# Kernel optimization log

Measured on AMD Instinct MI355X. Metric: run time of the kernel, lower is better.

## Reference

```python
import jax, jax.numpy as jnp
import numpy as np

B, S, D, H = 4, 2048, 512, 8
DH = D // H  # 64


def setup_inputs() -> dict:
    key = jax.random.key(0)
    ks = jax.random.split(key, 12)
    sc = 0.02
    return {
        "embed": jax.random.normal(ks[0], (B, S, D), dtype=jnp.float32),
        "Wq": jax.random.normal(ks[1], (H, DH, D), dtype=jnp.float32) * sc,
        "bq": jax.random.normal(ks[2], (H, DH), dtype=jnp.float32) * sc,
        "Wk": jax.random.normal(ks[3], (H, DH, D), dtype=jnp.float32) * sc,
        "bk": jax.random.normal(ks[4], (H, DH), dtype=jnp.float32) * sc,
        "Wv": jax.random.normal(ks[5], (H, DH, D), dtype=jnp.float32) * sc,
        "bv": jax.random.normal(ks[6], (H, DH), dtype=jnp.float32) * sc,
        "Wo": jax.random.normal(ks[7], (D, D), dtype=jnp.float32) * sc,
        "bo": jax.random.normal(ks[8], (D,), dtype=jnp.float32) * sc,
        "gamma": jnp.ones((D,), dtype=jnp.float32),
        "beta": jnp.zeros((D,), dtype=jnp.float32),
    }


def reference(embed, Wq, bq, Wk, bk, Wv, bv, Wo, bo, gamma, beta):
    # Per-head linear projections, vectorized over heads: [B,H,S,DH]
    q = jnp.einsum("bsd,hed->bhse", embed, Wq) + bq[None, :, None, :]
    k = jnp.einsum("bsd,hed->bhse", embed, Wk) + bk[None, :, None, :]
    v = jnp.einsum("bsd,hed->bhse", embed, Wv) + bv[None, :, None, :]

    # Full score matrix [B,H,S,S], tril applied to RAW scores (zeros, not -inf),
    # scaled by sqrt(embedding_dim) -- faithful to the original module's math.
    att = jnp.einsum("bhse,bhte->bhst", q, k)
    att = jnp.tril(att)
    att = att / jnp.sqrt(jnp.float32(D))
    att = jax.nn.softmax(att, axis=-1)

    out = jnp.einsum("bhst,bhte->bhse", att, v)  # [B,H,S,DH]
    # concat heads along feature dim -> [B,S,D]
    out = jnp.transpose(out, (0, 2, 1, 3)).reshape(B, S, D)

    x = out @ Wo.T + bo
    x = x + embed

    # LayerNorm over last dim
    mu = jnp.mean(x, axis=-1, keepdims=True)
    var = jnp.var(x, axis=-1, keepdims=True)
    x = (x - mu) / jnp.sqrt(var + 1e-5) * gamma + beta
    return x
```

## Files before the change

### kernel.cpp

```cpp
#include <hip/hip_runtime.h>
#include <hip/hip_bf16.h>


typedef __bf16 bf16;
typedef __bf16 bf16x8 __attribute__((ext_vector_type(8)));
typedef __bf16 bf16x4v __attribute__((ext_vector_type(4)));
typedef float f32x4 __attribute__((ext_vector_type(4)));

#define S_LEN 2048
#define DMODEL 512
#define QSCALE 0.06375870914f

#define GLDS(g, l) __builtin_amdgcn_global_load_lds(                  \
    (const __attribute__((address_space(1))) void*)(g),               \
    (__attribute__((address_space(3))) void*)(l), 16, 0, 0)

__global__ __launch_bounds__(256) void cast_all(
    const float* __restrict__ embed, const float* __restrict__ Wq,
    const float* __restrict__ Wk, const float* __restrict__ Wv,
    const float* __restrict__ Wo,
    bf16* __restrict__ Eb, bf16* __restrict__ Wqkv, bf16* __restrict__ Wob) {
  int i = blockIdx.x * 256 + threadIdx.x;
  const float* src;
  bf16* dst;
  int il;
  if (i < 1048576) {
    src = embed; dst = Eb; il = i;
  } else {
    int j = i - 1048576;
    int w = j >> 16;
    il = j & 65535;
    src = (w == 0) ? Wq : (w == 1) ? Wk : (w == 2) ? Wv : Wo;
    dst = (w == 3) ? Wob : Wqkv + (size_t)w * 262144;
  }
  float4 v = reinterpret_cast<const float4*>(src)[il];
  bf16x4v o;
  o[0] = (bf16)v.x; o[1] = (bf16)v.y; o[2] = (bf16)v.z; o[3] = (bf16)v.w;
  *reinterpret_cast<bf16x4v*>(dst + (size_t)il * 4) = o;
}

__device__ __forceinline__ void gemm128_core(
    const bf16* __restrict__ A, const bf16* __restrict__ Bw,
    int row0, int col0, bf16* As, bf16* Bs, f32x4 (&acc)[4][4]) {
  int tid = threadIdx.x;
  int w = tid >> 6, l = tid & 63, lr = l & 15, lg = l >> 4;
  int wr = w >> 1, wc = w & 1;

  int srow = w * 8 + (l >> 3);
  int scol = ((l & 7) ^ (srow & 7)) << 3;
  const bf16* ga = A + (size_t)(row0 + srow) * DMODEL + scol;
  const bf16* gb = Bw + (size_t)(col0 + srow) * DMODEL + scol;
  char* asb = (char*)As;
  char* bsb = (char*)Bs;
  int sbase = w * 1024;

  int aoff[4], boff[4];
#pragma unroll
  for (int m = 0; m < 4; ++m) {
    aoff[m] = (wr * 64 + m * 16 + lr) * 128 + (((lg ^ (lr & 7))) << 4);
    boff[m] = (wc * 64 + m * 16 + lr) * 128 + (((lg ^ (lr & 7))) << 4);
  }

  for (int k0 = 0; k0 < DMODEL; k0 += 64) {
#pragma unroll
    for (int qt = 0; qt < 4; ++qt) {
      GLDS(ga + (size_t)qt * 32 * DMODEL, asb + qt * 4096 + sbase);
      GLDS(gb + (size_t)qt * 32 * DMODEL, bsb + qt * 4096 + sbase);
    }
    ga += 64; gb += 64;
    __syncthreads();

    bf16x8 af[2][4], bfv[2][4];
#pragma unroll
    for (int m = 0; m < 4; ++m) {
      af[0][m] = *(const bf16x8*)(asb + aoff[m]);
      af[1][m] = *(const bf16x8*)(asb + (aoff[m] ^ 0x40));
      bfv[0][m] = *(const bf16x8*)(bsb + boff[m]);
      bfv[1][m] = *(const bf16x8*)(bsb + (boff[m] ^ 0x40));
    }
#pragma unroll
    for (int m = 0; m < 4; ++m)
#pragma unroll
      for (int n = 0; n < 4; ++n) {
        acc[m][n] = __builtin_amdgcn_mfma_f32_16x16x32_bf16(af[0][m], bfv[0][n], acc[m][n], 0, 0, 0);
        acc[m][n] = __builtin_amdgcn_mfma_f32_16x16x32_bf16(af[1][m], bfv[1][n], acc[m][n], 0, 0, 0);
      }
    __syncthreads();
  }
}

__global__ __launch_bounds__(256) void gemm_qkv(
    const bf16* __restrict__ A, const bf16* __restrict__ Wqkv,
    const float* __restrict__ bq, const float* __restrict__ bk, const float* __restrict__ bv,
    bf16* __restrict__ Qb, bf16* __restrict__ Kb, bf16* __restrict__ Vt) {
  __shared__ __align__(16) bf16 As[128 * 64];
  __shared__ __align__(16) bf16 Bs[128 * 64];
  int row0 = blockIdx.x * 128, col0 = blockIdx.y * 128;
  f32x4 acc[4][4] = {};
  gemm128_core(A, Wqkv, row0, col0, As, Bs, acc);

  int tid = threadIdx.x;
  int w = tid >> 6, l = tid & 63, lr = l & 15, lg = l >> 4;
  int wr = w >> 1, wc = w & 1;
  int z2 = col0 >> 9;
  if (z2 < 2) {
    bf16* O = z2 ? Kb : Qb;
    const float* bias = z2 ? bk : bq;
    float qs = z2 ? 1.0f : QSCALE;
#pragma unroll
    for (int n = 0; n < 4; ++n) {
      int cg = (col0 & 511) + wc * 64 + n * 16 + lr;
      float bi = bias[cg];
#pragma unroll
      for (int m = 0; m < 4; ++m) {
        int rg = row0 + wr * 64 + m * 16 + lg * 4;
#pragma unroll
        for (int r = 0; r < 4; ++r)
          O[(size_t)(rg + r) * DMODEL + cg] = (bf16)((acc[m][n][r] + bi) * qs);
      }
    }
  } else {
#pragma unroll
    for (int n = 0; n < 4; ++n) {
      int ep = (col0 & 511) + wc * 64 + n * 16 + lr;
      int h = ep >> 6, e = ep & 63;
      float bi = bv[ep];
#pragma unroll
      for (int m = 0; m < 4; ++m) {
        int rg = row0 + wr * 64 + m * 16 + lg * 4;
        int b = rg >> 11, s0 = rg & 2047;
        bf16x4v pk;
#pragma unroll
        for (int r = 0; r < 4; ++r) pk[r] = (bf16)(acc[m][n][r] + bi);
        *(bf16x4v*)(Vt + ((size_t)((b * 8 + h) * 64 + e)) * S_LEN + s0) = pk;
      }
    }
  }
}

__global__ __launch_bounds__(256) void gemm_wo(
    const bf16* __restrict__ A, const bf16* __restrict__ W,
    const float* __restrict__ bo, const float* __restrict__ embed,
    bf16* __restrict__ X) {
  __shared__ __align__(16) bf16 As[128 * 64];
  __shared__ __align__(16) bf16 Bs[128 * 64];
  int row0 = blockIdx.x * 128, col0 = blockIdx.y * 128;
  f32x4 acc[4][4] = {};
  gemm128_core(A, W, row0, col0, As, Bs, acc);

  int tid = threadIdx.x;
  int w = tid >> 6, l = tid & 63, lr = l & 15, lg = l >> 4;
  int wr = w >> 1, wc = w & 1;
#pragma unroll
  for (int n = 0; n < 4; ++n) {
    int cg = col0 + wc * 64 + n * 16 + lr;
    float bi = bo[cg];
#pragma unroll
    for (int m = 0; m < 4; ++m) {
      int rg = row0 + wr * 64 + m * 16 + lg * 4;
#pragma unroll
      for (int r = 0; r < 4; ++r)
        X[(size_t)(rg + r) * DMODEL + cg] =
            (bf16)(acc[m][n][r] + bi + embed[(size_t)(rg + r) * DMODEL + cg]);
    }
  }
}

__global__ __launch_bounds__(256) void suf_kernel(const bf16* __restrict__ Vt,
                                                  float* __restrict__ SUF) {
  int bh = blockIdx.x >> 3;
  int eg = blockIdx.x & 7;
  int el = threadIdx.x & 7;
  int seg = threadIdx.x >> 3;
  int e = eg * 8 + el;
  __shared__ float segtot[32][9];
  const bf16* vrow = Vt + ((size_t)bh * 64 + e) * S_LEN;
  float loc[4];
  float carry = 0.f;
#pragma unroll
  for (int j = 3; j >= 0; --j) {
    int jj = seg * 4 + j;
    bf16x8 a = *(const bf16x8*)(vrow + jj * 16);
    bf16x8 b2 = *(const bf16x8*)(vrow + jj * 16 + 8);
    float s = 0.f;
#pragma unroll
    for (int k = 0; k < 8; ++k) s += (float)a[k] + (float)b2[k];
    carry += s;
    loc[j] = carry;
  }
  segtot[seg][el] = carry;
  __syncthreads();
  float add = 0.f;
  for (int s2 = seg + 1; s2 < 32; ++s2) add += segtot[s2][el];
  float* srow = SUF + (size_t)bh * 129 * 64 + e;
#pragma unroll
  for (int j = 0; j < 4; ++j) srow[(size_t)(seg * 4 + j) * 64] = loc[j] + add;
  if (seg == 0) srow[(size_t)128 * 64] = 0.f;
}

__global__ __launch_bounds__(512) void flash_attn(
    const bf16* __restrict__ Qb, const bf16* __restrict__ Kb,
    const bf16* __restrict__ Vt, const float* __restrict__ SUF,
    bf16* __restrict__ attO) {
  int bh = blockIdx.y;
  int b = bh >> 3, h = bh & 7;
  int p = (int)gridDim.x - 1 - (int)blockIdx.x;
  int tid = threadIdx.x;
  int w = tid >> 6, l = tid & 63, lr = l & 15, lg = l >> 4;
  int wsub = w & 3;
  int qtile = (w < 4) ? (16 + p) : (15 - p);
  int qb = qtile * 64;
  int nt = 17 + p;

  __shared__ __align__(16) bf16 kl[3][64 * 64];
  __shared__ __align__(16) bf16 vl[3][64 * 64];
  __shared__ __align__(16) bf16 pl[8][16 * 64];

  int srow = qb + 16 * wsub + lr;
  const bf16* qptr = Qb + ((size_t)(b * S_LEN) + srow) * DMODEL + h * 64 + lg * 8;
  bf16x8 aq0 = *(const bf16x8*)(qptr);
  bf16x8 aq1 = *(const bf16x8*)(qptr + 32);

  float lsum[4] = {0.f, 0.f, 0.f, 0.f};
  f32x4 acc[4] = {};

  int tmax_w = qb + 16 * wsub + 16;

  int grow = tid >> 3, gch = tid & 7;
  int sch = ((gch ^ (grow & 7)) << 3);
  const bf16* Kg = Kb + ((size_t)(b * S_LEN) + grow) * DMODEL + h * 64 + sch;
  const bf16* Vg = Vt + ((size_t)(bh * 64) + grow) * S_LEN + sch;
  int sdst = w * 1024;

  int sw0 = (lg ^ (lr & 7)) << 4;
  int sw4 = sw0 ^ 0x40;
  char* plb = (char*)pl[w];

  GLDS(Kg, (char*)kl[0] + sdst);
  GLDS(Vg, (char*)vl[0] + sdst);
  GLDS(Kg + (size_t)64 * DMODEL, (char*)kl[1] + sdst);
  GLDS(Vg + 64, (char*)vl[1] + sdst);
  asm volatile("s_waitcnt vmcnt(2)" ::: "memory");
  __syncthreads();

  int cur = 0;
  for (int it = 0; it < nt; ++it) {
    int t0 = it << 6;
    bool more = (it + 2 < nt);
    if (more) {
      int stg = cur + 2; if (stg >= 3) stg -= 3;
      GLDS(Kg + (size_t)(t0 + 128) * DMODEL, (char*)kl[stg] + sdst);
      GLDS(Vg + (t0 + 128), (char*)vl[stg] + sdst);
    }
    if (t0 < tmax_w) {
      char* klb = (char*)kl[cur];
      char* vlb = (char*)vl[cur];

      f32x4 sfrag[4];
      const f32x4 fz = {0.f, 0.f, 0.f, 0.f};
      __builtin_amdgcn_s_setprio(1);
#pragma unroll
      for (int c = 0; c < 4; ++c) {
        int rb = (16 * c + lr) * 128;
        bf16x8 bk0 = *(const bf16x8*)(klb + rb + sw0);
        bf16x8 bk1 = *(const bf16x8*)(klb + rb + sw4);
        f32x4 t = __builtin_amdgcn_mfma_f32_16x16x32_bf16(aq0, bk0, fz, 0, 0, 0);
        sfrag[c] = __builtin_amdgcn_mfma_f32_16x16x32_bf16(aq1, bk1, t, 0, 0, 0);
      }
      __builtin_amdgcn_s_setprio(0);

      if (t0 + 64 <= qb + 16 * wsub) {
#pragma unroll
        for (int r = 0; r < 4; ++r) {
          int row = lg * 4 + r;
          int pbase = row * 128 + ((lr & 7) << 1);
          int xorv = row & 7;
          float psum = 0.f;
#pragma unroll
          for (int c = 0; c < 4; ++c) {
            float pv = exp2f(sfrag[c][r]);
            psum += pv;
            int chunk = 2 * c + (lr >> 3);
            *(bf16*)(plb + pbase + (((chunk ^ xorv) << 4))) = (bf16)pv;
          }
          lsum[r] += psum;
        }
      } else {
#pragma unroll
        for (int r = 0; r < 4; ++r) {
          int sg = qb + 16 * wsub + lg * 4 + r;
          int row = lg * 4 + r;
          int pbase = row * 128 + ((lr & 7) << 1);
          int xorv = row & 7;
          float psum = 0.f;
#pragma unroll
          for (int c = 0; c < 4; ++c) {
            int tg = t0 + 16 * c + lr;
            float x = (tg <= sg) ? sfrag[c][r] : ((tg < tmax_w) ? 0.f : -1e30f);
            float pv = exp2f(x);
            psum += pv;
            int chunk = 2 * c + (lr >> 3);
            *(bf16*)(plb + pbase + (((chunk ^ xorv) << 4))) = (bf16)pv;
          }
          lsum[r] += psum;
        }
      }

      bf16x8 pa0 = *(const bf16x8*)(plb + lr * 128 + sw0);
      bf16x8 pa1 = *(const bf16x8*)(plb + lr * 128 + sw4);
      __builtin_amdgcn_s_setprio(1);
#pragma unroll
      for (int c = 0; c < 4; ++c) {
        int rb = (16 * c + lr) * 128;
        bf16x8 bv0 = *(const bf16x8*)(vlb + rb + sw0);
        bf16x8 bv1 = *(const bf16x8*)(vlb + rb + sw4);
        acc[c] = __builtin_amdgcn_mfma_f32_16x16x32_bf16(pa0, bv0, acc[c], 0, 0, 0);
        acc[c] = __builtin_amdgcn_mfma_f32_16x16x32_bf16(pa1, bv1, acc[c], 0, 0, 0);
      }
      __builtin_amdgcn_s_setprio(0);
    }
    if (more) {
      asm volatile("s_waitcnt vmcnt(2)" ::: "memory");
    } else {
      asm volatile("s_waitcnt vmcnt(0)" ::: "memory");
    }
    __syncthreads();
    cur = (cur == 2) ? 0 : cur + 1;
  }

#pragma unroll
  for (int r = 0; r < 4; ++r) {
#pragma unroll
    for (int d = 1; d < 16; d <<= 1) lsum[r] += __shfl_xor(lsum[r], d, 64);
  }

  int j16 = tmax_w >> 4;
  const float* suf = SUF + ((size_t)bh * 129 + j16) * 64;
  float cnt = (float)(S_LEN - tmax_w);
  float sufe[4];
#pragma unroll
  for (int c = 0; c < 4; ++c) sufe[c] = suf[16 * c + lr];
#pragma unroll
  for (int r = 0; r < 4; ++r) {
    float inv = 1.f / (lsum[r] + cnt);
    int sg = qb + 16 * wsub + lg * 4 + r;
#pragma unroll
    for (int c = 0; c < 4; ++c) {
      float o = (acc[c][r] + sufe[c]) * inv;
      attO[((size_t)(b * S_LEN) + sg) * DMODEL + h * 64 + 16 * c + lr] = (bf16)o;
    }
  }
}

__global__ __launch_bounds__(256) void ln_kernel(const bf16* __restrict__ x,
                                                 const float* __restrict__ gamma,
                                                 const float* __restrict__ beta,
                                                 float* __restrict__ out) {
  int row = blockIdx.x * 4 + (threadIdx.x >> 6);
  int l = threadIdx.x & 63;
  bf16x8 xv = *(const bf16x8*)(x + (size_t)row * DMODEL + l * 8);
  float xf[8];
  float s = 0.f, s2 = 0.f;
#pragma unroll
  for (int k = 0; k < 8; ++k) {
    xf[k] = (float)xv[k];
    s += xf[k];
    s2 += xf[k] * xf[k];
  }
#pragma unroll
  for (int d = 1; d < 64; d <<= 1) {
    s += __shfl_xor(s, d, 64);
    s2 += __shfl_xor(s2, d, 64);
  }
  float mean = s * (1.f / 512.f);
  float var = s2 * (1.f / 512.f) - mean * mean;
  float rstd = rsqrtf(var + 1e-5f);
  const float4* g4 = reinterpret_cast<const float4*>(gamma) + l * 2;
  const float4* b4 = reinterpret_cast<const float4*>(beta) + l * 2;
  float4 g0 = g4[0], g1 = g4[1], bb0 = b4[0], bb1 = b4[1];
  float4 o0, o1;
  o0.x = (xf[0] - mean) * rstd * g0.x + bb0.x;
  o0.y = (xf[1] - mean) * rstd * g0.y + bb0.y;
  o0.z = (xf[2] - mean) * rstd * g0.z + bb0.z;
  o0.w = (xf[3] - mean) * rstd * g0.w + bb0.w;
  o1.x = (xf[4] - mean) * rstd * g1.x + bb1.x;
  o1.y = (xf[5] - mean) * rstd * g1.y + bb1.y;
  o1.z = (xf[6] - mean) * rstd * g1.z + bb1.z;
  o1.w = (xf[7] - mean) * rstd * g1.w + bb1.w;
  float4* orow = reinterpret_cast<float4*>(out + (size_t)row * DMODEL) + l * 2;
  orow[0] = o0;
  orow[1] = o1;
}

extern "C" void kernel_launch(void* const* d_in, const int* in_sizes, int n_in,
                              void* d_out, int out_size, void* d_ws, size_t ws_size,
                              hipStream_t stream) {
  const float* embed = (const float*)d_in[0];
  const float* Wq = (const float*)d_in[1];
  const float* bq = (const float*)d_in[2];
  const float* Wk = (const float*)d_in[3];
  const float* bk = (const float*)d_in[4];
  const float* Wv = (const float*)d_in[5];
  const float* bv = (const float*)d_in[6];
  const float* Wo = (const float*)d_in[7];
  const float* bo = (const float*)d_in[8];
  const float* gamma = (const float*)d_in[9];
  const float* beta = (const float*)d_in[10];
  float* out = (float*)d_out;

  char* ws = (char*)d_ws;
  size_t off = 0;
  auto alc = [&](size_t b) { size_t o = off; off += (b + 255) & ~(size_t)255; return o; };
  bf16* Eb    = (bf16*)(ws + alc(8192ull * 512 * 2));
  bf16* Wqkv  = (bf16*)(ws + alc(1536ull * 512 * 2));
  bf16* Wob   = (bf16*)(ws + alc(512ull * 512 * 2));
  bf16* Qb    = (bf16*)(ws + alc(8192ull * 512 * 2));
  bf16* Kb    = (bf16*)(ws + alc(8192ull * 512 * 2));
  bf16* Vt    = (bf16*)(ws + alc(8192ull * 512 * 2));
  float* SUF  = (float*)(ws + alc(32ull * 129 * 64 * 4));
  bf16* AttO  = (bf16*)(ws + alc(8192ull * 512 * 2));
  bf16* Xb    = (bf16*)(ws + alc(8192ull * 512 * 2));
  (void)ws_size; (void)n_in; (void)in_sizes; (void)out_size;

  cast_all<<<5120, 256, 0, stream>>>(embed, Wq, Wk, Wv, Wo, Eb, Wqkv, Wob);

  gemm_qkv<<<dim3(64, 12), 256, 0, stream>>>(Eb, Wqkv, bq, bk, bv, Qb, Kb, Vt);
  suf_kernel<<<256, 256, 0, stream>>>(Vt, SUF);
  flash_attn<<<dim3(16, 32), 512, 0, stream>>>(Qb, Kb, Vt, SUF, AttO);
  gemm_wo<<<dim3(64, 4), 256, 0, stream>>>(AttO, Wob, bo, embed, Xb);
  ln_kernel<<<2048, 256, 0, stream>>>(Xb, gamma, beta, out);
}
```

Baseline: 106.6 us.

## Halve attention block to 4 waves each handling 32 query rows

The flash attention kernel now uses 256 threads per block, and each wave processes two 16-row query sub-tiles instead of one. Each K/V fragment read from LDS is therefore reused for twice as many MFMAs, cutting LDS traffic per FLOP. The K/V ring drops from triple to double buffering with a full vmcnt(0) wait each iteration, and launch bounds request 3 blocks per CU. The trade-off is higher register pressure and less prefetch depth, so load latency may be exposed. Causal masking is also coarser per wave, which adds some wasted work.

```diff
diff --git a/kernel.cpp b/kernel.cpp
--- a/kernel.cpp
+++ b/kernel.cpp
@@ -198,33 +198,31 @@
   if (seg == 0) srow[(size_t)128 * 64] = 0.f;
 }
 
-__global__ __launch_bounds__(512) void flash_attn(
+__global__ __launch_bounds__(256, 3) void flash_attn(
     const bf16* __restrict__ Qb, const bf16* __restrict__ Kb,
     const bf16* __restrict__ Vt, const float* __restrict__ SUF,
     bf16* __restrict__ attO) {
   int bh = blockIdx.y;
   int b = bh >> 3, h = bh & 7;
-  int p = (int)gridDim.x - 1 - (int)blockIdx.x;
+  int p = 15 - (int)blockIdx.x;
   int tid = threadIdx.x;
   int w = tid >> 6, l = tid & 63, lr = l & 15, lg = l >> 4;
-  int wsub = w & 3;
-  int qtile = (w < 4) ? (16 + p) : (15 - p);
-  int qb = qtile * 64;
+  int qbase = (w < 2) ? ((16 + p) * 64 + w * 32) : ((15 - p) * 64 + (w - 2) * 32);
   int nt = 17 + p;
-
-  __shared__ __align__(16) bf16 kl[3][64 * 64];
-  __shared__ __align__(16) bf16 vl[3][64 * 64];
-  __shared__ __align__(16) bf16 pl[8][16 * 64];
-
-  int srow = qb + 16 * wsub + lr;
-  const bf16* qptr = Qb + ((size_t)(b * S_LEN) + srow) * DMODEL + h * 64 + lg * 8;
-  bf16x8 aq0 = *(const bf16x8*)(qptr);
-  bf16x8 aq1 = *(const bf16x8*)(qptr + 32);
-
-  float lsum[4] = {0.f, 0.f, 0.f, 0.f};
-  f32x4 acc[4] = {};
-
-  int tmax_w = qb + 16 * wsub + 16;
+  int ntw = (qbase >> 6) + 1;
+
+  __shared__ __align__(16) bf16 kl[2][64 * 64];
+  __shared__ __align__(16) bf16 vl[2][64 * 64];
+  __shared__ __align__(16) bf16 pl[4][2][16 * 64];
+
+  const bf16* qp = Qb + ((size_t)(b * S_LEN) + qbase + lr) * DMODEL + h * 64 + lg * 8;
+  bf16x8 aq00 = *(const bf16x8*)(qp);
+  bf16x8 aq01 = *(const bf16x8*)(qp + 32);
+  bf16x8 aq10 = *(const bf16x8*)(qp + 16 * DMODEL);
+  bf16x8 aq11 = *(const bf16x8*)(qp + 16 * DMODEL + 32);
+
+  float lsum0[4] = {}, lsum1[4] = {};
+  f32x4 acc0[4] = {}, acc1[4] = {};
 
   int grow = tid >> 3, gch = tid & 7;
   int sch = ((gch ^ (grow & 7)) << 3);
@@ -234,29 +232,30 @@
 
   int sw0 = (lg ^ (lr & 7)) << 4;
   int sw4 = sw0 ^ 0x40;
-  char* plb = (char*)pl[w];
+  char* plb0 = (char*)pl[w][0];
+  char* plb1 = (char*)pl[w][1];
 
   GLDS(Kg, (char*)kl[0] + sdst);
+  GLDS(Kg + (size_t)32 * DMODEL, (char*)kl[0] + 4096 + sdst);
   GLDS(Vg, (char*)vl[0] + sdst);
-  GLDS(Kg + (size_t)64 * DMODEL, (char*)kl[1] + sdst);
-  GLDS(Vg + 64, (char*)vl[1] + sdst);
-  asm volatile("s_waitcnt vmcnt(2)" ::: "memory");
+  GLDS(Vg + (size_t)32 * S_LEN, (char*)vl[0] + 4096 + sdst);
+  asm volatile("s_waitcnt vmcnt(0)" ::: "memory");
   __syncthreads();
 
   int cur = 0;
   for (int it = 0; it < nt; ++it) {
     int t0 = it << 6;
-    bool more = (it + 2 < nt);
-    if (more) {
-      int stg = cur + 2; if (stg >= 3) stg -= 3;
-      GLDS(Kg + (size_t)(t0 + 128) * DMODEL, (char*)kl[stg] + sdst);
-      GLDS(Vg + (t0 + 128), (char*)vl[stg] + sdst);
-    }
-    if (t0 < tmax_w) {
+    if (it + 1 < nt) {
+      GLDS(Kg + (size_t)(t0 + 64) * DMODEL, (char*)kl[cur ^ 1] + sdst);
+      GLDS(Kg + (size_t)(t0 + 96) * DMODEL, (char*)kl[cur ^ 1] + 4096 + sdst);
+      GLDS(Vg + (t0 + 64), (char*)vl[cur ^ 1] + sdst);
+      GLDS(Vg + (size_t)32 * S_LEN + (t0 + 64), (char*)vl[cur ^ 1] + 4096 + sdst);
+    }
+    if (it < ntw) {
       char* klb = (char*)kl[cur];
       char* vlb = (char*)vl[cur];
 
-      f32x4 sfrag[4];
+      f32x4 sf0[4], sf1[4];
       const f32x4 fz = {0.f, 0.f, 0.f, 0.f};
       __builtin_amdgcn_s_setprio(1);
 #pragma unroll
@@ -264,90 +263,108 @@
         int rb = (16 * c + lr) * 128;
         bf16x8 bk0 = *(const bf16x8*)(klb + rb + sw0);
         bf16x8 bk1 = *(const bf16x8*)(klb + rb + sw4);
-        f32x4 t = __builtin_amdgcn_mfma_f32_16x16x32_bf16(aq0, bk0, fz, 0, 0, 0);
-        sfrag[c] = __builtin_amdgcn_mfma_f32_16x16x32_bf16(aq1, bk1, t, 0, 0, 0);
+        f32x4 t = __builtin_amdgcn_mfma_f32_16x16x32_bf16(aq00, bk0, fz, 0, 0, 0);
+        sf0[c] = __builtin_amdgcn_mfma_f32_16x16x32_bf16(aq01, bk1, t, 0, 0, 0);
+        f32x4 t2 = __builtin_amdgcn_mfma_f32_16x16x32_bf16(aq10, bk0, fz, 0, 0, 0);
+        sf1[c] = __builtin_amdgcn_mfma_f32_16x16x32_bf16(aq11, bk1, t2, 0, 0, 0);
       }
       __builtin_amdgcn_s_setprio(0);
 
-      if (t0 + 64 <= qb + 16 * wsub) {
+      if (it + 1 < ntw) {
 #pragma unroll
         for (int r = 0; r < 4; ++r) {
           int row = lg * 4 + r;
           int pbase = row * 128 + ((lr & 7) << 1);
           int xorv = row & 7;
-          float psum = 0.f;
+          float ps0 = 0.f, ps1 = 0.f;
 #pragma unroll
           for (int c = 0; c < 4; ++c) {
-            float pv = exp2f(sfrag[c][r]);
-            psum += pv;
-            int chunk = 2 * c + (lr >> 3);
-            *(bf16*)(plb + pbase + (((chunk ^ xorv) << 4))) = (bf16)pv;
+            int soff = ((2 * c + (lr >> 3)) ^ xorv) << 4;
+            float pv0 = exp2f(sf0[c][r]);
+            float pv1 = exp2f(sf1[c][r]);
+            ps0 += pv0; ps1 += pv1;
+            *(bf16*)(plb0 + pbase + soff) = (bf16)pv0;
+            *(bf16*)(plb1 + pbase + soff) = (bf16)pv1;
           }
-          lsum[r] += psum;
+          lsum0[r] += ps0; lsum1[r] += ps1;
         }
       } else {
 #pragma unroll
         for (int r = 0; r < 4; ++r) {
-          int sg = qb + 16 * wsub + lg * 4 + r;
           int row = lg * 4 + r;
           int pbase = row * 128 + ((lr & 7) << 1);
           int xorv = row & 7;
-          float psum = 0.f;
+          int sg0 = qbase + lg * 4 + r;
+          int sg1 = sg0 + 16;
+          int tmax0 = qbase + 16, tmax1 = qbase + 32;
+          float ps0 = 0.f, ps1 = 0.f;
 #pragma unroll
           for (int c = 0; c < 4; ++c) {
             int tg = t0 + 16 * c + lr;
-            float x = (tg <= sg) ? sfrag[c][r] : ((tg < tmax_w) ? 0.f : -1e30f);
-            float pv = exp2f(x);
-            psum += pv;
-            int chunk = 2 * c + (lr >> 3);
-            *(bf16*)(plb + pbase + (((chunk ^ xorv) << 4))) = (bf16)pv;
+            float x0 = (tg <= sg0) ? sf0[c][r] : ((tg < tmax0) ? 0.f : -1e30f);
+            float x1 = (tg <= sg1) ? sf1[c][r] : ((tg < tmax1) ? 0.f : -1e30f);
+            float pv0 = exp2f(x0);
+            float pv1 = exp2f(x1);
+            ps0 += pv0; ps1 += pv1;
+            int soff = ((2 * c + (lr >> 3)) ^ xorv) << 4;
+            *(bf16*)(plb0 + pbase + soff) = (bf16)pv0;
+            *(bf16*)(plb1 + pbase + soff) = (bf16)pv1;
           }
-          lsum[r] += psum;
+          lsum0[r] += ps0; lsum1[r] += ps1;
         }
       }
 
-      bf16x8 pa0 = *(const bf16x8*)(plb + lr * 128 + sw0);
-      bf16x8 pa1 = *(const bf16x8*)(plb + lr * 128 + sw4);
+      bf16x8 pa00 = *(const bf16x8*)(plb0 + lr * 128 + sw0);
+      bf16x8 pa01 = *(const bf16x8*)(plb0 + lr * 128 + sw4);
+      bf16x8 pa10 = *(const bf16x8*)(plb1 + lr * 128 + sw0);
+      bf16x8 pa11 = *(const bf16x8*)(plb1 + lr * 128 + sw4);
       __builtin_amdgcn_s_setprio(1);
 #pragma unroll
       for (int c = 0; c < 4; ++c) {
         int rb = (16 * c + lr) * 128;
         bf16x8 bv0 = *(const bf16x8*)(vlb + rb + sw0);
         bf16x8 bv1 = *(const bf16x8*)(vlb + rb + sw4);
-        acc[c] = __builtin_amdgcn_mfma_f32_16x16x32_bf16(pa0, bv0, acc[c], 0, 0, 0);
-        acc[c] = __builtin_amdgcn_mfma_f32_16x16x32_bf16(pa1, bv1, acc[c], 0, 0, 0);
+        acc0[c] = __builtin_amdgcn_mfma_f32_16x16x32_bf16(pa00, bv0, acc0[c], 0, 0, 0);
+        acc0[c] = __builtin_amdgcn_mfma_f32_16x16x32_bf16(pa01, bv1, acc0[c], 0, 0, 0);
+        acc1[c] = __builtin_amdgcn_mfma_f32_16x16x32_bf16(pa10, bv0, acc1[c], 0, 0, 0);
+        acc1[c] = __builtin_amdgcn_mfma_f32_16x16x32_bf16(pa11, bv1, acc1[c], 0, 0, 0);
       }
       __builtin_amdgcn_s_setprio(0);
     }
-    if (more) {
-      asm volatile("s_waitcnt vmcnt(2)" ::: "memory");
-    } else {
-      asm volatile("s_waitcnt vmcnt(0)" ::: "memory");
-    }
+    asm volatile("s_waitcnt vmcnt(0)" ::: "memory");
     __syncthreads();
-    cur = (cur == 2) ? 0 : cur + 1;
+    cur ^= 1;
   }
 
 #pragma unroll
   for (int r = 0; r < 4; ++r) {
 #pragma unroll
-    for (int d = 1; d < 16; d <<= 1) lsum[r] += __shfl_xor(lsum[r], d, 64);
-  }
-
-  int j16 = tmax_w >> 4;
-  const float* suf = SUF + ((size_t)bh * 129 + j16) * 64;
-  float cnt = (float)(S_LEN - tmax_w);
-  float sufe[4];
-#pragma unroll
-  for (int c = 0; c < 4; ++c) sufe[c] = suf[16 * c + lr];
-#pragma unroll
-  for (int r = 0; r < 4; ++r) {
-    float inv = 1.f / (lsum[r] + cnt);
-    int sg = qb + 16 * wsub + lg * 4 + r;
-#pragma unroll
-    for (int c = 0; c < 4; ++c) {
-      float o = (acc[c][r] + sufe[c]) * inv;
-      attO[((size_t)(b * S_LEN) + sg) * DMODEL + h * 64 + 16 * c + lr] = (bf16)o;
+    for (int d = 1; d < 16; d <<= 1) {
+      lsum0[r] += __shfl_xor(lsum0[r], d, 64);
+      lsum1[r] += __shfl_xor(lsum1[r], d, 64);
+    }
+  }
+
+#pragma unroll
+  for (int s = 0; s < 2; ++s) {
+    int row0s = qbase + 16 * s;
+    int j16 = (row0s + 16) >> 4;
+    const float* suf = SUF + ((size_t)bh * 129 + j16) * 64;
+    float cnt = (float)(S_LEN - (row0s + 16));
+    float sufe[4];
+#pragma unroll
+    for (int c = 0; c < 4; ++c) sufe[c] = suf[16 * c + lr];
+#pragma unroll
+    for (int r = 0; r < 4; ++r) {
+      float ls = s ? lsum1[r] : lsum0[r];
+      float inv = 1.f / (ls + cnt);
+      int sg = row0s + lg * 4 + r;
+#pragma unroll
+      for (int c = 0; c < 4; ++c) {
+        float a = s ? acc1[c][r] : acc0[c][r];
+        attO[((size_t)(b * S_LEN) + sg) * DMODEL + h * 64 + 16 * c + lr] =
+            (bf16)((a + sufe[c]) * inv);
+      }
     }
   }
 }
@@ -426,7 +443,7 @@
 
   gemm_qkv<<<dim3(64, 12), 256, 0, stream>>>(Eb, Wqkv, bq, bk, bv, Qb, Kb, Vt);
   suf_kernel<<<256, 256, 0, stream>>>(Vt, SUF);
-  flash_attn<<<dim3(16, 32), 512, 0, stream>>>(Qb, Kb, Vt, SUF, AttO);
+  flash_attn<<<dim3(16, 32), 256, 0, stream>>>(Qb, Kb, Vt, SUF, AttO);
   gemm_wo<<<dim3(64, 4), 256, 0, stream>>>(AttO, Wob, bo, embed, Xb);
   ln_kernel<<<2048, 256, 0, stream>>>(Xb, gamma, beta, out);
 }
```

New measurement: 122.8 us. +15.3%, slower.

## Process 128-key tiles per iteration with double buffering in flash attention

Applied to the files above, without the earlier changes.

The attention loop now consumes 128 keys per iteration instead of 64. It switches from a 3-stage, 64-row ring buffer to a 2-stage double buffer of 128-row K and V tiles, which halves the number of barriers and loop iterations. Each iteration waits for all outstanding loads (vmcnt(0)) rather than keeping one tile in flight, so load latency is hidden less deeply. Each wave computes scores for 8 column chunks when both halves are needed and then runs the P·V step per 64-key half.

```diff
diff --git a/kernel.cpp b/kernel.cpp
--- a/kernel.cpp
+++ b/kernel.cpp
@@ -210,21 +210,21 @@
   int wsub = w & 3;
   int qtile = (w < 4) ? (16 + p) : (15 - p);
   int qb = qtile * 64;
-  int nt = 17 + p;
-
-  __shared__ __align__(16) bf16 kl[3][64 * 64];
-  __shared__ __align__(16) bf16 vl[3][64 * 64];
+  int qbw = qb + 16 * wsub;
+  int tmax_w = qbw + 16;
+  int nt = (18 + p) >> 1;
+  int ntw = (tmax_w + 127) >> 7;
+
+  __shared__ __align__(16) bf16 kl[2][128 * 64];
+  __shared__ __align__(16) bf16 vl[2][2][64 * 64];
   __shared__ __align__(16) bf16 pl[8][16 * 64];
 
-  int srow = qb + 16 * wsub + lr;
-  const bf16* qptr = Qb + ((size_t)(b * S_LEN) + srow) * DMODEL + h * 64 + lg * 8;
+  const bf16* qptr = Qb + ((size_t)(b * S_LEN) + qbw + lr) * DMODEL + h * 64 + lg * 8;
   bf16x8 aq0 = *(const bf16x8*)(qptr);
   bf16x8 aq1 = *(const bf16x8*)(qptr + 32);
 
   float lsum[4] = {0.f, 0.f, 0.f, 0.f};
   f32x4 acc[4] = {};
-
-  int tmax_w = qb + 16 * wsub + 16;
 
   int grow = tid >> 3, gch = tid & 7;
   int sch = ((gch ^ (grow & 7)) << 3);
@@ -237,95 +237,101 @@
   char* plb = (char*)pl[w];
 
   GLDS(Kg, (char*)kl[0] + sdst);
-  GLDS(Vg, (char*)vl[0] + sdst);
-  GLDS(Kg + (size_t)64 * DMODEL, (char*)kl[1] + sdst);
-  GLDS(Vg + 64, (char*)vl[1] + sdst);
-  asm volatile("s_waitcnt vmcnt(2)" ::: "memory");
+  GLDS(Kg + (size_t)64 * DMODEL, (char*)kl[0] + 8192 + sdst);
+  GLDS(Vg, (char*)vl[0][0] + sdst);
+  GLDS(Vg + 64, (char*)vl[0][1] + sdst);
+  asm volatile("s_waitcnt vmcnt(0)" ::: "memory");
   __syncthreads();
 
   int cur = 0;
   for (int it = 0; it < nt; ++it) {
-    int t0 = it << 6;
-    bool more = (it + 2 < nt);
-    if (more) {
-      int stg = cur + 2; if (stg >= 3) stg -= 3;
-      GLDS(Kg + (size_t)(t0 + 128) * DMODEL, (char*)kl[stg] + sdst);
-      GLDS(Vg + (t0 + 128), (char*)vl[stg] + sdst);
-    }
-    if (t0 < tmax_w) {
+    int t0 = it << 7;
+    if (it + 1 < nt) {
+      GLDS(Kg + (size_t)(t0 + 128) * DMODEL, (char*)kl[cur ^ 1] + sdst);
+      GLDS(Kg + (size_t)(t0 + 192) * DMODEL, (char*)kl[cur ^ 1] + 8192 + sdst);
+      GLDS(Vg + (t0 + 128), (char*)vl[cur ^ 1][0] + sdst);
+      GLDS(Vg + (t0 + 192), (char*)vl[cur ^ 1][1] + sdst);
+    }
+    if (it < ntw) {
       char* klb = (char*)kl[cur];
-      char* vlb = (char*)vl[cur];
-
-      f32x4 sfrag[4];
+      bool ph1 = (t0 + 64) < tmax_w;
+
+      f32x4 sf[8];
       const f32x4 fz = {0.f, 0.f, 0.f, 0.f};
+      int ncq = ph1 ? 8 : 4;
       __builtin_amdgcn_s_setprio(1);
-#pragma unroll
-      for (int c = 0; c < 4; ++c) {
-        int rb = (16 * c + lr) * 128;
-        bf16x8 bk0 = *(const bf16x8*)(klb + rb + sw0);
-        bf16x8 bk1 = *(const bf16x8*)(klb + rb + sw4);
-        f32x4 t = __builtin_amdgcn_mfma_f32_16x16x32_bf16(aq0, bk0, fz, 0, 0, 0);
-        sfrag[c] = __builtin_amdgcn_mfma_f32_16x16x32_bf16(aq1, bk1, t, 0, 0, 0);
+#pragma unroll 8
+      for (int c = 0; c < 8; ++c) {
+        if (c < ncq) {
+          int rb = (16 * c + lr) * 128;
+          bf16x8 bk0 = *(const bf16x8*)(klb + rb + sw0);
+          bf16x8 bk1 = *(const bf16x8*)(klb + rb + sw4);
+          f32x4 t = __builtin_amdgcn_mfma_f32_16x16x32_bf16(aq0, bk0, fz, 0, 0, 0);
+          sf[c] = __builtin_amdgcn_mfma_f32_16x16x32_bf16(aq1, bk1, t, 0, 0, 0);
+        }
       }
       __builtin_amdgcn_s_setprio(0);
 
-      if (t0 + 64 <= qb + 16 * wsub) {
-#pragma unroll
-        for (int r = 0; r < 4; ++r) {
-          int row = lg * 4 + r;
-          int pbase = row * 128 + ((lr & 7) << 1);
-          int xorv = row & 7;
-          float psum = 0.f;
-#pragma unroll
-          for (int c = 0; c < 4; ++c) {
-            float pv = exp2f(sfrag[c][r]);
-            psum += pv;
-            int chunk = 2 * c + (lr >> 3);
-            *(bf16*)(plb + pbase + (((chunk ^ xorv) << 4))) = (bf16)pv;
+#pragma unroll
+      for (int hp = 0; hp < 2; ++hp) {
+        int t0p = t0 + 64 * hp;
+        if (hp == 1 && !ph1) break;
+        char* vlb = (char*)vl[cur][hp];
+
+        if (t0p + 64 <= qbw) {
+#pragma unroll
+          for (int r = 0; r < 4; ++r) {
+            int row = lg * 4 + r;
+            int pbase = row * 128 + ((lr & 7) << 1);
+            int xorv = row & 7;
+            float psum = 0.f;
+#pragma unroll
+            for (int c = 0; c < 4; ++c) {
+              float pv = exp2f(sf[4 * hp + c][r]);
+              psum += pv;
+              int chunk = 2 * c + (lr >> 3);
+              *(bf16*)(plb + pbase + (((chunk ^ xorv) << 4))) = (bf16)pv;
+            }
+            lsum[r] += psum;
           }
-          lsum[r] += psum;
+        } else {
+#pragma unroll
+          for (int r = 0; r < 4; ++r) {
+            int sg = qbw + lg * 4 + r;
+            int row = lg * 4 + r;
+            int pbase = row * 128 + ((lr & 7) << 1);
+            int xorv = row & 7;
+            float psum = 0.f;
+#pragma unroll
+            for (int c = 0; c < 4; ++c) {
+              int tg = t0p + 16 * c + lr;
+              float x = (tg <= sg) ? sf[4 * hp + c][r] : ((tg < tmax_w) ? 0.f : -1e30f);
+              float pv = exp2f(x);
+              psum += pv;
+              int chunk = 2 * c + (lr >> 3);
+              *(bf16*)(plb + pbase + (((chunk ^ xorv) << 4))) = (bf16)pv;
+            }
+            lsum[r] += psum;
+          }
         }
-      } else {
-#pragma unroll
-        for (int r = 0; r < 4; ++r) {
-          int sg = qb + 16 * wsub + lg * 4 + r;
-          int row = lg * 4 + r;
-          int pbase = row * 128 + ((lr & 7) << 1);
-          int xorv = row & 7;
-          float psum = 0.f;
-#pragma unroll
-          for (int c = 0; c < 4; ++c) {
-            int tg = t0 + 16 * c + lr;
-            float x = (tg <= sg) ? sfrag[c][r] : ((tg < tmax_w) ? 0.f : -1e30f);
-            float pv = exp2f(x);
-            psum += pv;
-            int chunk = 2 * c + (lr >> 3);
-            *(bf16*)(plb + pbase + (((chunk ^ xorv) << 4))) = (bf16)pv;
-          }
-          lsum[r] += psum;
+
+        bf16x8 pa0 = *(const bf16x8*)(plb + lr * 128 + sw0);
+        bf16x8 pa1 = *(const bf16x8*)(plb + lr * 128 + sw4);
+        __builtin_amdgcn_s_setprio(1);
+#pragma unroll
+        for (int c = 0; c < 4; ++c) {
+          int rb = (16 * c + lr) * 128;
+          bf16x8 bv0 = *(const bf16x8*)(vlb + rb + sw0);
+          bf16x8 bv1 = *(const bf16x8*)(vlb + rb + sw4);
+          acc[c] = __builtin_amdgcn_mfma_f32_16x16x32_bf16(pa0, bv0, acc[c], 0, 0, 0);
+          acc[c] = __builtin_amdgcn_mfma_f32_16x16x32_bf16(pa1, bv1, acc[c], 0, 0, 0);
         }
+        __builtin_amdgcn_s_setprio(0);
       }
-
-      bf16x8 pa0 = *(const bf16x8*)(plb + lr * 128 + sw0);
-      bf16x8 pa1 = *(const bf16x8*)(plb + lr * 128 + sw4);
-      __builtin_amdgcn_s_setprio(1);
-#pragma unroll
-      for (int c = 0; c < 4; ++c) {
-        int rb = (16 * c + lr) * 128;
-        bf16x8 bv0 = *(const bf16x8*)(vlb + rb + sw0);
-        bf16x8 bv1 = *(const bf16x8*)(vlb + rb + sw4);
-        acc[c] = __builtin_amdgcn_mfma_f32_16x16x32_bf16(pa0, bv0, acc[c], 0, 0, 0);
-        acc[c] = __builtin_amdgcn_mfma_f32_16x16x32_bf16(pa1, bv1, acc[c], 0, 0, 0);
-      }
-      __builtin_amdgcn_s_setprio(0);
-    }
-    if (more) {
-      asm volatile("s_waitcnt vmcnt(2)" ::: "memory");
-    } else {
-      asm volatile("s_waitcnt vmcnt(0)" ::: "memory");
-    }
+    }
+    asm volatile("s_waitcnt vmcnt(0)" ::: "memory");
     __syncthreads();
-    cur = (cur == 2) ? 0 : cur + 1;
+    cur ^= 1;
   }
 
 #pragma unroll
@@ -343,7 +349,7 @@
 #pragma unroll
   for (int r = 0; r < 4; ++r) {
     float inv = 1.f / (lsum[r] + cnt);
-    int sg = qb + 16 * wsub + lg * 4 + r;
+    int sg = qbw + lg * 4 + r;
 #pragma unroll
     for (int c = 0; c < 4; ++c) {
       float o = (acc[c][r] + sufe[c]) * inv;
```

Measured after the change: 101.6 us. -4.6%, faster.
